# Kernel optimization log

Measured on AMD Instinct MI355X. Metric: run time of the kernel, lower is better.

Reference implementation:

```python
import jax, jax.numpy as jnp
import numpy as np

H, E, NI = 100000, 200000, 1000000
D_H, D_E, D_OUT = 128, 64, 128
LN_EPS = 1e-5


def _linear(x, W, b):
    # torch nn.Linear convention: W is [out, in]
    return x @ W.T + b


def _scatter_mean(vals, idx, num_segments):
    # scatter_mean with empty segments producing 0 (sum=0 / max(count,1))
    s = jax.ops.segment_sum(vals, idx, num_segments=num_segments)
    c = jax.ops.segment_sum(jnp.ones((vals.shape[0], 1), vals.dtype), idx,
                            num_segments=num_segments)
    return s / jnp.maximum(c, 1.0)


def setup_inputs() -> dict:
    key = jax.random.key(0)
    ks = jax.random.split(key, 16)
    inv = lambda n: 1.0 / np.sqrt(n)
    return {
        "x_h": jax.random.normal(ks[0], (H, D_H), jnp.float32),
        "h2_edge_attr": jax.random.normal(ks[1], (E, D_E), jnp.float32),
        "Wp": jax.random.uniform(ks[2], (D_OUT, D_H), jnp.float32, -inv(D_H), inv(D_H)),
        "bp": jnp.zeros((D_OUT,), jnp.float32),
        "We1": jax.random.uniform(ks[3], (D_OUT, D_H + D_E), jnp.float32, -inv(D_H + D_E), inv(D_H + D_E)),
        "be1": jnp.zeros((D_OUT,), jnp.float32),
        "We2": jax.random.uniform(ks[4], (D_OUT, D_OUT), jnp.float32, -inv(D_OUT), inv(D_OUT)),
        "be2": jnp.zeros((D_OUT,), jnp.float32),
        "Wn1": jax.random.uniform(ks[5], (D_OUT, D_OUT), jnp.float32, -inv(D_OUT), inv(D_OUT)),
        "bn1": jnp.zeros((D_OUT,), jnp.float32),
        "Wn2": jax.random.uniform(ks[6], (D_OUT, D_OUT), jnp.float32, -inv(D_OUT), inv(D_OUT)),
        "bn2": jnp.zeros((D_OUT,), jnp.float32),
        "gamma": jnp.ones((D_OUT,), jnp.float32),
        "beta": jnp.zeros((D_OUT,), jnp.float32),
        "fg_id": jax.random.randint(ks[7], (NI,), 0, H, jnp.int32),
        "res_id": jax.random.randint(ks[8], (NI,), 0, E, jnp.int32),
    }


def reference(x_h, h2_edge_attr, Wp, bp, We1, be1, We2, be2,
              Wn1, bn1, Wn2, bn2, gamma, beta, fg_id, res_id):
    # node -> edge: mean of member node features per hyperedge
    edge_node_mean = _scatter_mean(x_h[fg_id], res_id, E)            # [E, d_h]
    e_in = jnp.concatenate([edge_node_mean, h2_edge_attr], axis=-1)  # [E, d_h+d_e]
    edge_msg = _linear(jax.nn.relu(_linear(e_in, We1, be1)), We2, be2)  # [E, d_out]
    # edge -> node: mean of incident edge messages per hypernode
    node_msg = _scatter_mean(edge_msg[res_id], fg_id, H)             # [H, d_out]
    z = _linear(x_h, Wp, bp) + _linear(jax.nn.relu(_linear(node_msg, Wn1, bn1)), Wn2, bn2)
    z = jax.nn.relu(z)
    mu = jnp.mean(z, axis=-1, keepdims=True)
    var = jnp.var(z, axis=-1, keepdims=True)
    return (z - mu) * jax.lax.rsqrt(var + LN_EPS) * gamma + beta
```

## Files before the change

### kernel.cpp

```cpp
#include <hip/hip_runtime.h>

#define H_N   100000
#define E_N   200000
#define NI_N  1000000
#define LN_EPS 1e-5f

#define NBUCK_E 3125
#define NBUCK_H 1563
#define SUBCAP_E 128
#define SUBCAP_H 192
#define CAP_E 512
#define CAP_H 1024
#define BCNT_PAD 16

typedef __attribute__((ext_vector_type(8))) short bf16x8;
typedef __attribute__((ext_vector_type(4))) float floatx4;
typedef __attribute__((ext_vector_type(4))) int intx4;
typedef __attribute__((ext_vector_type(4))) unsigned uintx4;

__device__ inline unsigned short f2bf(float f) {
  unsigned u = __builtin_bit_cast(unsigned, f);
  u += 0x7fffu + ((u >> 16) & 1u);
  return (unsigned short)(u >> 16);
}
__device__ inline float bf2f(unsigned short s) {
  unsigned u = ((unsigned)s) << 16;
  return __builtin_bit_cast(float, u);
}
__device__ inline unsigned get_xcc() {
  unsigned x;
  asm volatile("s_getreg_b32 %0, hwreg(HW_REG_XCC_ID)" : "=s"(x));
  return x & 7;
}

__global__ __launch_bounds__(256) void k_cvt_bf16(const float4* __restrict__ src,
                                                  unsigned short* __restrict__ dst,
                                                  int n4) {
  int i = blockIdx.x * 256 + threadIdx.x;
  if (i >= n4) return;
  float4 v = src[i];
  union { unsigned short us[4]; unsigned long long u64; } p;
  p.us[0] = f2bf(v.x); p.us[1] = f2bf(v.y);
  p.us[2] = f2bf(v.z); p.us[3] = f2bf(v.w);
  *(unsigned long long*)(dst + (size_t)i * 4) = p.u64;
}

__global__ __launch_bounds__(256) void k_bucket(
    const int* __restrict__ fg, const int* __restrict__ res,
    int* __restrict__ bcnt_e, int* __restrict__ bcnt_h,
    unsigned* __restrict__ pairs_e, unsigned* __restrict__ pairs_h) {
  int i0 = (blockIdx.x * 256 + threadIdx.x) * 4;
  if (i0 >= NI_N) return;
  unsigned xcc = get_xcc();
  intx4 f4 = __builtin_nontemporal_load((const intx4*)(fg + i0));
  intx4 r4 = __builtin_nontemporal_load((const intx4*)(res + i0));
#pragma unroll
  for (int j = 0; j < 4; ++j) {
    int f = f4[j], r = r4[j];
    int be = r >> 6, se = r & 63;
    int pe = atomicAdd(bcnt_e + ((size_t)xcc * NBUCK_E + be) * BCNT_PAD, 1);
    if (pe < SUBCAP_E)
      pairs_e[((size_t)xcc * NBUCK_E + be) * SUBCAP_E + pe] =
          ((unsigned)se << 24) | (unsigned)f;
    int bh = f >> 6, sh = f & 63;
    int ph = atomicAdd(bcnt_h + ((size_t)xcc * NBUCK_H + bh) * BCNT_PAD, 1);
    if (ph < SUBCAP_H)
      pairs_h[((size_t)xcc * NBUCK_H + bh) * SUBCAP_H + ph] =
          ((unsigned)sh << 24) | (unsigned)r;
  }
}

#define GATHER_QW(basePtr)                                                     \
  for (int s = wave; s < 64; s += 4) {                                         \
    int o = cnts[s], e = cnts[s + 1];                                          \
    float a[8];                                                                \
    _Pragma("unroll")                                                          \
    for (int k = 0; k < 8; ++k) a[k] = 0.f;                                    \
    int j = o + q;                                                             \
    for (; j + 4 < e; j += 8) {                                                \
      unsigned off0 = sortedp[j], off1 = sortedp[j + 4];                       \
      uintx4 v0 = *(const uintx4*)((const char*)(basePtr) + off0 + ql * 16);   \
      uintx4 v1 = *(const uintx4*)((const char*)(basePtr) + off1 + ql * 16);   \
      _Pragma("unroll")                                                        \
      for (int k = 0; k < 4; ++k) {                                            \
        a[2 * k]     += bf2f((unsigned short)(v0[k] & 0xffffu)) +              \
                        bf2f((unsigned short)(v1[k] & 0xffffu));               \
        a[2 * k + 1] += bf2f((unsigned short)(v0[k] >> 16)) +                  \
                        bf2f((unsigned short)(v1[k] >> 16));                   \
      }                                                                        \
    }                                                                          \
    if (j < e) {                                                               \
      unsigned off0 = sortedp[j];                                              \
      uintx4 v0 = *(const uintx4*)((const char*)(basePtr) + off0 + ql * 16);   \
      _Pragma("unroll")                                                        \
      for (int k = 0; k < 4; ++k) {                                            \
        a[2 * k]     += bf2f((unsigned short)(v0[k] & 0xffffu));               \
        a[2 * k + 1] += bf2f((unsigned short)(v0[k] >> 16));                   \
      }                                                                        \
    }                                                                          \
    _Pragma("unroll")                                                          \
    for (int k = 0; k < 8; ++k) {                                              \
      a[k] += __shfl_xor(a[k], 16, 64);                                        \
      a[k] += __shfl_xor(a[k], 32, 64);                                        \
    }                                                                          \
    if (q == 0) {                                                              \
      float inv = (e > o) ? 1.0f / (float)(e - o) : 0.0f;                      \
      uintx4 ov;                                                               \
      _Pragma("unroll")                                                        \
      for (int k = 0; k < 4; ++k)                                              \
        ov[k] = (unsigned)f2bf(a[2 * k] * inv) |                               \
                ((unsigned)f2bf(a[2 * k + 1] * inv) << 16);                    \
      *(uintx4*)&meanS[s][ql * 8] = ov;                                        \
    }                                                                          \
  }

__global__ __launch_bounds__(256, 6) void k_edge_fused(
    const unsigned short* __restrict__ xh, const short* __restrict__ attr_bf,
    const unsigned* __restrict__ pairs, const int* __restrict__ bcnt,
    const short* __restrict__ w1, const float* __restrict__ b1,
    const short* __restrict__ w2, const float* __restrict__ b2,
    unsigned short* __restrict__ edge_msg) {
  __shared__ short meanS[64][136];
  __shared__ unsigned raw[CAP_E];
  __shared__ unsigned sortedp[CAP_E];
  __shared__ int cnts[65];
  __shared__ int curs[64];
  short (*h1s)[136] = meanS;

  const int b = blockIdx.x;
  const int t = threadIdx.x;

  int total = 0;
#pragma unroll
  for (int x = 0; x < 8; ++x) {
    int c = min(bcnt[((size_t)x * NBUCK_E + b) * BCNT_PAD], SUBCAP_E);
    const unsigned* src = pairs + ((size_t)x * NBUCK_E + b) * SUBCAP_E;
    for (int j = t; j < c; j += 256) {
      int d = total + j;
      if (d < CAP_E) raw[d] = src[j];
    }
    total += c;
  }
  const int cnt = min(total, CAP_E);
  if (t <= 64) cnts[t] = 0;
  __syncthreads();
  for (int j = t; j < cnt; j += 256)
    atomicAdd(&cnts[(raw[j] >> 24) + 1], 1);
  __syncthreads();
  for (int d = 1; d <= 64; d <<= 1) {
    int v = 0;
    if (t <= 64 && t >= d) v = cnts[t - d];
    __syncthreads();
    if (t <= 64) cnts[t] += v;
    __syncthreads();
  }
  if (t < 64) curs[t] = cnts[t];
  __syncthreads();
  for (int j = t; j < cnt; j += 256) {
    unsigned p = raw[j];
    int d = atomicAdd(&curs[p >> 24], 1);
    sortedp[d] = (p & 0xFFFFFFu) << 8;
  }
  __syncthreads();

  const int wave = t >> 6, lane = t & 63;
  const int q = lane >> 4, ql = lane & 15;
  GATHER_QW(xh);
  __syncthreads();

  const int row  = lane & 15;
  const int quad = lane >> 4;
  const int e0   = b * 64;
  const int cb   = wave * 32;

  bf16x8 B1[2][6];
#pragma unroll
  for (int nl = 0; nl < 2; ++nl)
#pragma unroll
    for (int ks = 0; ks < 6; ++ks)
      B1[nl][ks] = *(const bf16x8*)(w1 + (size_t)(cb + nl * 16 + row) * 192 +
                                    ks * 32 + quad * 8);

  floatx4 acc[4][2];
#pragma unroll
  for (int m = 0; m < 4; ++m)
#pragma unroll
    for (int nl = 0; nl < 2; ++nl) acc[m][nl] = (floatx4){0.f, 0.f, 0.f, 0.f};

#pragma unroll
  for (int ks = 0; ks < 6; ++ks) {
    bf16x8 a[4];
#pragma unroll
    for (int m = 0; m < 4; ++m) {
      if (ks < 4) {
        a[m] = *(const bf16x8*)&meanS[m * 16 + row][ks * 32 + quad * 8];
      } else {
        int e = e0 + m * 16 + row;
        a[m] = *(const bf16x8*)(attr_bf + (size_t)e * 64 + (ks - 4) * 32 + quad * 8);
      }
    }
#pragma unroll
    for (int m = 0; m < 4; ++m)
#pragma unroll
      for (int nl = 0; nl < 2; ++nl)
        acc[m][nl] = __builtin_amdgcn_mfma_f32_16x16x32_bf16(a[m], B1[nl][ks],
                                                             acc[m][nl], 0, 0, 0);
  }
  __syncthreads();

#pragma unroll
  for (int nl = 0; nl < 2; ++nl) {
    float bias = b1[cb + nl * 16 + row];
#pragma unroll
    for (int m = 0; m < 4; ++m)
#pragma unroll
      for (int r = 0; r < 4; ++r)
        h1s[m * 16 + quad * 4 + r][cb + nl * 16 + row] =
            (short)f2bf(fmaxf(acc[m][nl][r] + bias, 0.0f));
  }

  bf16x8 B2[2][4];
#pragma unroll
  for (int nl = 0; nl < 2; ++nl)
#pragma unroll
    for (int ks = 0; ks < 4; ++ks)
      B2[nl][ks] = *(const bf16x8*)(w2 + (size_t)(cb + nl * 16 + row) * 128 +
                                    ks * 32 + quad * 8);
  __syncthreads();

  floatx4 acc2[4][2];
#pragma unroll
  for (int m = 0; m < 4; ++m)
#pragma unroll
    for (int nl = 0; nl < 2; ++nl) acc2[m][nl] = (floatx4){0.f, 0.f, 0.f, 0.f};

#pragma unroll
  for (int ks = 0; ks < 4; ++ks) {
    bf16x8 a[4];
#pragma unroll
    for (int m = 0; m < 4; ++m)
      a[m] = *(const bf16x8*)&h1s[m * 16 + row][ks * 32 + quad * 8];
#pragma unroll
    for (int m = 0; m < 4; ++m)
#pragma unroll
      for (int nl = 0; nl < 2; ++nl)
        acc2[m][nl] = __builtin_amdgcn_mfma_f32_16x16x32_bf16(a[m], B2[nl][ks],
                                                              acc2[m][nl], 0, 0, 0);
  }

#pragma unroll
  for (int nl = 0; nl < 2; ++nl) {
    int col = cb + nl * 16 + row;
    float bias = b2[col];
#pragma unroll
    for (int m = 0; m < 4; ++m)
#pragma unroll
      for (int r = 0; r < 4; ++r)
        edge_msg[(size_t)(e0 + m * 16 + quad * 4 + r) * 128 + col] =
            f2bf(acc2[m][nl][r] + bias);
  }
}

__global__ __launch_bounds__(256, 5) void k_node_fused(
    const unsigned short* __restrict__ emsg, const short* __restrict__ xh_bf,
    const unsigned* __restrict__ pairs, const int* __restrict__ bcnt,
    const short* __restrict__ wp, const float* __restrict__ bp,
    const short* __restrict__ wn1, const float* __restrict__ bn1,
    const short* __restrict__ wn2, const float* __restrict__ bn2,
    const float* __restrict__ gamma, const float* __restrict__ beta,
    float* __restrict__ out) {
  __shared__ short meanS[64][136];
  __shared__ unsigned raw[CAP_H];
  __shared__ unsigned sortedp[CAP_H];
  __shared__ int cnts[65];
  __shared__ int curs[64];
  short (*h1s)[136] = meanS;
  float2 (*part)[4] = (float2(*)[4])raw;

  const int b = blockIdx.x;
  const int t = threadIdx.x;

  int total = 0;
#pragma unroll
  for (int x = 0; x < 8; ++x) {
    int c = min(bcnt[((size_t)x * NBUCK_H + b) * BCNT_PAD], SUBCAP_H);
    const unsigned* src = pairs + ((size_t)x * NBUCK_H + b) * SUBCAP_H;
    for (int j = t; j < c; j += 256) {
      int d = total + j;
      if (d < CAP_H) raw[d] = src[j];
    }
    total += c;
  }
  const int cnt = min(total, CAP_H);
  if (t <= 64) cnts[t] = 0;
  __syncthreads();
  for (int j = t; j < cnt; j += 256)
    atomicAdd(&cnts[(raw[j] >> 24) + 1], 1);
  __syncthreads();
  for (int d = 1; d <= 64; d <<= 1) {
    int v = 0;
    if (t <= 64 && t >= d) v = cnts[t - d];
    __syncthreads();
    if (t <= 64) cnts[t] += v;
    __syncthreads();
  }
  if (t < 64) curs[t] = cnts[t];
  __syncthreads();
  for (int j = t; j < cnt; j += 256) {
    unsigned p = raw[j];
    int d = atomicAdd(&curs[p >> 24], 1);
    sortedp[d] = (p & 0xFFFFFFu) << 8;
  }
  __syncthreads();

  const int wave = t >> 6, lane = t & 63;
  const int q = lane >> 4, ql = lane & 15;
  const int segs_here = min(64, H_N - b * 64);
  GATHER_QW(emsg);
  (void)segs_here;
  __syncthreads();

  const int row  = lane & 15;
  const int quad = lane >> 4;
  const int n0   = b * 64;
  const int cb   = wave * 32;

  bf16x8 B1[2][4];
#pragma unroll
  for (int nl = 0; nl < 2; ++nl)
#pragma unroll
    for (int ks = 0; ks < 4; ++ks)
      B1[nl][ks] = *(const bf16x8*)(wn1 + (size_t)(cb + nl * 16 + row) * 128 +
                                    ks * 32 + quad * 8);

  floatx4 acc[4][2];
#pragma unroll
  for (int m = 0; m < 4; ++m)
#pragma unroll
    for (int nl = 0; nl < 2; ++nl) acc[m][nl] = (floatx4){0.f, 0.f, 0.f, 0.f};

#pragma unroll
  for (int ks = 0; ks < 4; ++ks) {
    bf16x8 a[4];
#pragma unroll
    for (int m = 0; m < 4; ++m)
      a[m] = *(const bf16x8*)&meanS[m * 16 + row][ks * 32 + quad * 8];
#pragma unroll
    for (int m = 0; m < 4; ++m)
#pragma unroll
      for (int nl = 0; nl < 2; ++nl)
        acc[m][nl] = __builtin_amdgcn_mfma_f32_16x16x32_bf16(a[m], B1[nl][ks],
                                                             acc[m][nl], 0, 0, 0);
  }
  __syncthreads();

#pragma unroll
  for (int nl = 0; nl < 2; ++nl) {
    float bias = bn1[cb + nl * 16 + row];
#pragma unroll
    for (int m = 0; m < 4; ++m)
#pragma unroll
      for (int r = 0; r < 4; ++r)
        h1s[m * 16 + quad * 4 + r][cb + nl * 16 + row] =
            (short)f2bf(fmaxf(acc[m][nl][r] + bias, 0.0f));
  }

  bf16x8 B2[2][4], Bp[2][4];
#pragma unroll
  for (int nl = 0; nl < 2; ++nl)
#pragma unroll
    for (int ks = 0; ks < 4; ++ks) {
      B2[nl][ks] = *(const bf16x8*)(wn2 + (size_t)(cb + nl * 16 + row) * 128 +
                                    ks * 32 + quad * 8);
      Bp[nl][ks] = *(const bf16x8*)(wp + (size_t)(cb + nl * 16 + row) * 128 +
                                    ks * 32 + quad * 8);
    }
  __syncthreads();

  floatx4 acc2[4][2];
#pragma unroll
  for (int m = 0; m < 4; ++m)
#pragma unroll
    for (int nl = 0; nl < 2; ++nl) acc2[m][nl] = (floatx4){0.f, 0.f, 0.f, 0.f};

#pragma unroll
  for (int ks = 0; ks < 4; ++ks) {
    bf16x8 at[4], ax[4];
#pragma unroll
    for (int m = 0; m < 4; ++m) {
      at[m] = *(const bf16x8*)&h1s[m * 16 + row][ks * 32 + quad * 8];
      int n = n0 + m * 16 + row;
      ax[m] = *(const bf16x8*)(xh_bf + (size_t)n * 128 + ks * 32 + quad * 8);
    }
#pragma unroll
    for (int m = 0; m < 4; ++m)
#pragma unroll
      for (int nl = 0; nl < 2; ++nl) {
        acc2[m][nl] = __builtin_amdgcn_mfma_f32_16x16x32_bf16(at[m], B2[nl][ks],
                                                              acc2[m][nl], 0, 0, 0);
        acc2[m][nl] = __builtin_amdgcn_mfma_f32_16x16x32_bf16(ax[m], Bp[nl][ks],
                                                              acc2[m][nl], 0, 0, 0);
      }
  }

  float z[4][2][4];
#pragma unroll
  for (int m = 0; m < 4; ++m) {
    float s[4], ss[4];
#pragma unroll
    for (int r = 0; r < 4; ++r) { s[r] = 0.f; ss[r] = 0.f; }
#pragma unroll
    for (int nl = 0; nl < 2; ++nl) {
      float bias = bp[cb + nl * 16 + row] + bn2[cb + nl * 16 + row];
#pragma unroll
      for (int r = 0; r < 4; ++r) {
        float v = fmaxf(acc2[m][nl][r] + bias, 0.0f);
        z[m][nl][r] = v;
        s[r] += v;
        ss[r] += v * v;
      }
    }
#pragma unroll
    for (int r = 0; r < 4; ++r) {
#pragma unroll
      for (int msk = 1; msk < 16; msk <<= 1) {
        s[r]  += __shfl_xor(s[r],  msk, 64);
        ss[r] += __shfl_xor(ss[r], msk, 64);
      }
      if (row == 0) part[m * 16 + quad * 4 + r][wave] = make_float2(s[r], ss[r]);
    }
  }
  __syncthreads();

#pragma unroll
  for (int m = 0; m < 4; ++m)
#pragma unroll
    for (int r = 0; r < 4; ++r) {
      int rr = m * 16 + quad * 4 + r;
      float2 p0 = part[rr][0], p1 = part[rr][1], p2 = part[rr][2], p3 = part[rr][3];
      float mean = (p0.x + p1.x + p2.x + p3.x) * (1.0f / 128.0f);
      float var  = (p0.y + p1.y + p2.y + p3.y) * (1.0f / 128.0f) - mean * mean;
      float rstd = rsqrtf(var + LN_EPS);
      int n = n0 + rr;
      if (n < H_N) {
#pragma unroll
        for (int nl = 0; nl < 2; ++nl) {
          int col = cb + nl * 16 + row;
          out[(size_t)n * 128 + col] =
              (z[m][nl][r] - mean) * rstd * gamma[col] + beta[col];
        }
      }
    }
}

extern "C" void kernel_launch(void* const* d_in, const int* in_sizes, int n_in,
                              void* d_out, int out_size, void* d_ws, size_t ws_size,
                              hipStream_t stream) {
  const float* x_h   = (const float*)d_in[0];
  const float* attr  = (const float*)d_in[1];
  const float* Wp    = (const float*)d_in[2];
  const float* bp    = (const float*)d_in[3];
  const float* We1   = (const float*)d_in[4];
  const float* be1   = (const float*)d_in[5];
  const float* We2   = (const float*)d_in[6];
  const float* be2   = (const float*)d_in[7];
  const float* Wn1   = (const float*)d_in[8];
  const float* bn1   = (const float*)d_in[9];
  const float* Wn2   = (const float*)d_in[10];
  const float* bn2   = (const float*)d_in[11];
  const float* gamma = (const float*)d_in[12];
  const float* beta  = (const float*)d_in[13];
  const int*   fg    = (const int*)d_in[14];
  const int*   res   = (const int*)d_in[15];
  float* out = (float*)d_out;

  int* bcnt_e = (int*)d_ws;
  int* bcnt_h = bcnt_e + (size_t)8 * NBUCK_E * BCNT_PAD;
  unsigned* pairs_e = (unsigned*)(bcnt_h + (size_t)8 * NBUCK_H * BCNT_PAD);
  unsigned* pairs_h = pairs_e + (size_t)8 * NBUCK_E * SUBCAP_E;
  unsigned short* xh_bf    = (unsigned short*)(pairs_h + (size_t)8 * NBUCK_H * SUBCAP_H);
  unsigned short* edge_msg = xh_bf + (size_t)H_N * 128;
  short* w1  = (short*)(edge_msg + (size_t)E_N * 128);
  short* w2  = w1 + 128 * 192;
  short* wn1 = w2 + 128 * 128;
  short* wn2 = wn1 + 128 * 128;
  short* wp  = wn2 + 128 * 128;
  short* attr_bf = wp + 128 * 128;

  hipMemsetAsync(bcnt_e, 0,
                 (size_t)(8 * NBUCK_E + 8 * NBUCK_H) * BCNT_PAD * 4, stream);

  {
    int n4 = H_N * 128 / 4;
    k_cvt_bf16<<<(n4 + 255) / 256, 256, 0, stream>>>((const float4*)x_h, xh_bf, n4);
    n4 = E_N * 64 / 4;
    k_cvt_bf16<<<(n4 + 255) / 256, 256, 0, stream>>>((const float4*)attr, (unsigned short*)attr_bf, n4);
    n4 = 128 * 192 / 4;
    k_cvt_bf16<<<(n4 + 255) / 256, 256, 0, stream>>>((const float4*)We1, (unsigned short*)w1, n4);
    n4 = 128 * 128 / 4;
    k_cvt_bf16<<<(n4 + 255) / 256, 256, 0, stream>>>((const float4*)We2, (unsigned short*)w2, n4);
    k_cvt_bf16<<<(n4 + 255) / 256, 256, 0, stream>>>((const float4*)Wn1, (unsigned short*)wn1, n4);
    k_cvt_bf16<<<(n4 + 255) / 256, 256, 0, stream>>>((const float4*)Wn2, (unsigned short*)wn2, n4);
    k_cvt_bf16<<<(n4 + 255) / 256, 256, 0, stream>>>((const float4*)Wp, (unsigned short*)wp, n4);
  }

  k_bucket<<<(NI_N / 4 + 255) / 256, 256, 0, stream>>>(fg, res, bcnt_e, bcnt_h,
                                                       pairs_e, pairs_h);

  k_edge_fused<<<NBUCK_E, 256, 0, stream>>>(xh_bf, attr_bf, pairs_e, bcnt_e,
                                            w1, be1, w2, be2, edge_msg);
  k_node_fused<<<NBUCK_H, 256, 0, stream>>>(edge_msg, (const short*)xh_bf,
                                            pairs_h, bcnt_h,
                                            wp, bp, wn1, bn1, wn2, bn2,
                                            gamma, beta, out);
}
```

Before: 476.2 us.

## Fuse conversion launches and memset into one prep kernel, restructure segment gather

After: 459.8 us (median of 2 runs). -3.4%, faster.

```diff
diff --git a/kernel.cpp b/kernel.cpp
--- a/kernel.cpp
+++ b/kernel.cpp
@@ -33,16 +33,74 @@
   return x & 7;
 }
 
-__global__ __launch_bounds__(256) void k_cvt_bf16(const float4* __restrict__ src,
-                                                  unsigned short* __restrict__ dst,
-                                                  int n4) {
-  int i = blockIdx.x * 256 + threadIdx.x;
+#define PREP_XH_BLKS   12500
+#define PREP_ATTR_BLKS 12500
+#define PREP_W1_BLKS   24
+#define PREP_W_BLKS    16
+#define PREP_ZERO_BLKS 586
+#define PREP_TOTAL (PREP_XH_BLKS + PREP_ATTR_BLKS + PREP_W1_BLKS + 4*PREP_W_BLKS + PREP_ZERO_BLKS)
+
+__device__ inline void cvt4(const float4* __restrict__ src,
+                            unsigned short* __restrict__ dst, int i, int n4) {
   if (i >= n4) return;
   float4 v = src[i];
   union { unsigned short us[4]; unsigned long long u64; } p;
   p.us[0] = f2bf(v.x); p.us[1] = f2bf(v.y);
   p.us[2] = f2bf(v.z); p.us[3] = f2bf(v.w);
   *(unsigned long long*)(dst + (size_t)i * 4) = p.u64;
+}
+
+__global__ __launch_bounds__(256) void k_prep(
+    const float4* __restrict__ x_h, unsigned short* __restrict__ xh_bf,
+    const float4* __restrict__ attr, unsigned short* __restrict__ attr_bf,
+    const float4* __restrict__ We1, unsigned short* __restrict__ w1,
+    const float4* __restrict__ We2, unsigned short* __restrict__ w2,
+    const float4* __restrict__ Wn1, unsigned short* __restrict__ wn1,
+    const float4* __restrict__ Wn2, unsigned short* __restrict__ wn2,
+    const float4* __restrict__ Wp, unsigned short* __restrict__ wp,
+    intx4* __restrict__ bcnt_zero) {
+  int blk = blockIdx.x;
+  int tid = threadIdx.x;
+  if (blk < PREP_XH_BLKS) {
+    cvt4(x_h, xh_bf, blk * 256 + tid, H_N * 128 / 4);
+    return;
+  }
+  blk -= PREP_XH_BLKS;
+  if (blk < PREP_ATTR_BLKS) {
+    cvt4(attr, attr_bf, blk * 256 + tid, E_N * 64 / 4);
+    return;
+  }
+  blk -= PREP_ATTR_BLKS;
+  if (blk < PREP_W1_BLKS) {
+    cvt4(We1, w1, blk * 256 + tid, 128 * 192 / 4);
+    return;
+  }
+  blk -= PREP_W1_BLKS;
+  if (blk < PREP_W_BLKS) {
+    cvt4(We2, w2, blk * 256 + tid, 128 * 128 / 4);
+    return;
+  }
+  blk -= PREP_W_BLKS;
+  if (blk < PREP_W_BLKS) {
+    cvt4(Wn1, wn1, blk * 256 + tid, 128 * 128 / 4);
+    return;
+  }
+  blk -= PREP_W_BLKS;
+  if (blk < PREP_W_BLKS) {
+    cvt4(Wn2, wn2, blk * 256 + tid, 128 * 128 / 4);
+    return;
+  }
+  blk -= PREP_W_BLKS;
+  if (blk < PREP_W_BLKS) {
+    cvt4(Wp, wp, blk * 256 + tid, 128 * 128 / 4);
+    return;
+  }
+  blk -= PREP_W_BLKS;
+  {
+    int i = blk * 256 + tid;
+    int n = (8 * NBUCK_E + 8 * NBUCK_H) * BCNT_PAD / 4;
+    if (i < n) bcnt_zero[i] = (intx4){0, 0, 0, 0};
+  }
 }
 
 __global__ __launch_bounds__(256) void k_bucket(
@@ -60,56 +118,53 @@
     int be = r >> 6, se = r & 63;
     int pe = atomicAdd(bcnt_e + ((size_t)xcc * NBUCK_E + be) * BCNT_PAD, 1);
     if (pe < SUBCAP_E)
-      pairs_e[((size_t)xcc * NBUCK_E + be) * SUBCAP_E + pe] =
-          ((unsigned)se << 24) | (unsigned)f;
+      __builtin_nontemporal_store(((unsigned)se << 24) | (unsigned)f,
+          &pairs_e[((size_t)xcc * NBUCK_E + be) * SUBCAP_E + pe]);
     int bh = f >> 6, sh = f & 63;
     int ph = atomicAdd(bcnt_h + ((size_t)xcc * NBUCK_H + bh) * BCNT_PAD, 1);
     if (ph < SUBCAP_H)
-      pairs_h[((size_t)xcc * NBUCK_H + bh) * SUBCAP_H + ph] =
-          ((unsigned)sh << 24) | (unsigned)r;
-  }
-}
-
-#define GATHER_QW(basePtr)                                                     \
-  for (int s = wave; s < 64; s += 4) {                                         \
-    int o = cnts[s], e = cnts[s + 1];                                          \
-    float a[8];                                                                \
-    _Pragma("unroll")                                                          \
-    for (int k = 0; k < 8; ++k) a[k] = 0.f;                                    \
-    int j = o + q;                                                             \
-    for (; j + 4 < e; j += 8) {                                                \
-      unsigned off0 = sortedp[j], off1 = sortedp[j + 4];                       \
-      uintx4 v0 = *(const uintx4*)((const char*)(basePtr) + off0 + ql * 16);   \
-      uintx4 v1 = *(const uintx4*)((const char*)(basePtr) + off1 + ql * 16);   \
+      __builtin_nontemporal_store(((unsigned)sh << 24) | (unsigned)r,
+          &pairs_h[((size_t)xcc * NBUCK_H + bh) * SUBCAP_H + ph]);
+  }
+}
+
+#define GATHER_QSEG(basePtr)                                                   \
+  {                                                                            \
+    const int qid = (t >> 4);                                                  \
+    for (int k = 0; k < 4; ++k) {                                              \
+      int s = qid + 16 * k;                                                    \
+      int o = cnts[s], e = cnts[s + 1];                                        \
+      float a[8];                                                              \
       _Pragma("unroll")                                                        \
-      for (int k = 0; k < 4; ++k) {                                            \
-        a[2 * k]     += bf2f((unsigned short)(v0[k] & 0xffffu)) +              \
-                        bf2f((unsigned short)(v1[k] & 0xffffu));               \
-        a[2 * k + 1] += bf2f((unsigned short)(v0[k] >> 16)) +                  \
-                        bf2f((unsigned short)(v1[k] >> 16));                   \
+      for (int x = 0; x < 8; ++x) a[x] = 0.f;                                  \
+      int j = o;                                                               \
+      for (; j + 1 < e; j += 2) {                                              \
+        unsigned off0 = sortedp[j], off1 = sortedp[j + 1];                     \
+        uintx4 v0 = *(const uintx4*)((const char*)(basePtr) + off0 + ql * 16); \
+        uintx4 v1 = *(const uintx4*)((const char*)(basePtr) + off1 + ql * 16); \
+        _Pragma("unroll")                                                      \
+        for (int x = 0; x < 4; ++x) {                                          \
+          a[2 * x]     += bf2f((unsigned short)(v0[x] & 0xffffu)) +            \
+                          bf2f((unsigned short)(v1[x] & 0xffffu));             \
+          a[2 * x + 1] += bf2f((unsigned short)(v0[x] >> 16)) +                \
+                          bf2f((unsigned short)(v1[x] >> 16));                 \
+        }                                                                      \
       }                                                                        \
-    }                                                                          \
-    if (j < e) {                                                               \
-      unsigned off0 = sortedp[j];                                              \
-      uintx4 v0 = *(const uintx4*)((const char*)(basePtr) + off0 + ql * 16);   \
-      _Pragma("unroll")                                                        \
-      for (int k = 0; k < 4; ++k) {                                            \
-        a[2 * k]     += bf2f((unsigned short)(v0[k] & 0xffffu));               \
-        a[2 * k + 1] += bf2f((unsigned short)(v0[k] >> 16));                   \
+      if (j < e) {                                                             \
+        unsigned off0 = sortedp[j];                                            \
+        uintx4 v0 = *(const uintx4*)((const char*)(basePtr) + off0 + ql * 16); \
+        _Pragma("unroll")                                                      \
+        for (int x = 0; x < 4; ++x) {                                          \
+          a[2 * x]     += bf2f((unsigned short)(v0[x] & 0xffffu));             \
+          a[2 * x + 1] += bf2f((unsigned short)(v0[x] >> 16));                 \
+        }                                                                      \
       }                                                                        \
-    }                                                                          \
-    _Pragma("unroll")                                                          \
-    for (int k = 0; k < 8; ++k) {                                              \
-      a[k] += __shfl_xor(a[k], 16, 64);                                        \
-      a[k] += __shfl_xor(a[k], 32, 64);                                        \
-    }                                                                          \
-    if (q == 0) {                                                              \
       float inv = (e > o) ? 1.0f / (float)(e - o) : 0.0f;                      \
       uintx4 ov;                                                               \
       _Pragma("unroll")                                                        \
-      for (int k = 0; k < 4; ++k)                                              \
-        ov[k] = (unsigned)f2bf(a[2 * k] * inv) |                               \
-                ((unsigned)f2bf(a[2 * k + 1] * inv) << 16);                    \
+      for (int x = 0; x < 4; ++x)                                              \
+        ov[x] = (unsigned)f2bf(a[2 * x] * inv) |                               \
+                ((unsigned)f2bf(a[2 * x + 1] * inv) << 16);                    \
       *(uintx4*)&meanS[s][ql * 8] = ov;                                        \
     }                                                                          \
   }
@@ -164,8 +219,8 @@
   __syncthreads();
 
   const int wave = t >> 6, lane = t & 63;
-  const int q = lane >> 4, ql = lane & 15;
-  GATHER_QW(xh);
+  const int ql = lane & 15;
+  GATHER_QSEG(xh);
   __syncthreads();
 
   const int row  = lane & 15;
@@ -314,10 +369,8 @@
   __syncthreads();
 
   const int wave = t >> 6, lane = t & 63;
-  const int q = lane >> 4, ql = lane & 15;
-  const int segs_here = min(64, H_N - b * 64);
-  GATHER_QW(emsg);
-  (void)segs_here;
+  const int ql = lane & 15;
+  GATHER_QSEG(emsg);
   __syncthreads();
 
   const int row  = lane & 15;
@@ -487,22 +540,15 @@
   short* wp  = wn2 + 128 * 128;
   short* attr_bf = wp + 128 * 128;
 
-  hipMemsetAsync(bcnt_e, 0,
-                 (size_t)(8 * NBUCK_E + 8 * NBUCK_H) * BCNT_PAD * 4, stream);
-
-  {
-    int n4 = H_N * 128 / 4;
-    k_cvt_bf16<<<(n4 + 255) / 256, 256, 0, stream>>>((const float4*)x_h, xh_bf, n4);
-    n4 = E_N * 64 / 4;
-    k_cvt_bf16<<<(n4 + 255) / 256, 256, 0, stream>>>((const float4*)attr, (unsigned short*)attr_bf, n4);
-    n4 = 128 * 192 / 4;
-    k_cvt_bf16<<<(n4 + 255) / 256, 256, 0, stream>>>((const float4*)We1, (unsigned short*)w1, n4);
-    n4 = 128 * 128 / 4;
-    k_cvt_bf16<<<(n4 + 255) / 256, 256, 0, stream>>>((const float4*)We2, (unsigned short*)w2, n4);
-    k_cvt_bf16<<<(n4 + 255) / 256, 256, 0, stream>>>((const float4*)Wn1, (unsigned short*)wn1, n4);
-    k_cvt_bf16<<<(n4 + 255) / 256, 256, 0, stream>>>((const float4*)Wn2, (unsigned short*)wn2, n4);
-    k_cvt_bf16<<<(n4 + 255) / 256, 256, 0, stream>>>((const float4*)Wp, (unsigned short*)wp, n4);
-  }
+  k_prep<<<PREP_TOTAL, 256, 0, stream>>>(
+      (const float4*)x_h, xh_bf,
+      (const float4*)attr, (unsigned short*)attr_bf,
+      (const float4*)We1, (unsigned short*)w1,
+      (const float4*)We2, (unsigned short*)w2,
+      (const float4*)Wn1, (unsigned short*)wn1,
+      (const float4*)Wn2, (unsigned short*)wn2,
+      (const float4*)Wp, (unsigned short*)wp,
+      (intx4*)bcnt_e);
 
   k_bucket<<<(NI_N / 4 + 255) / 256, 256, 0, stream>>>(fg, res, bcnt_e, bcnt_h,
                                                        pairs_e, pairs_h);
```
